# Kernel tuning notes

Hardware: AMD Instinct MI355X
Metric: run time of the kernel (lower is better)

The kernel has to match this reference:

```python
import jax, jax.numpy as jnp
import numpy as np

N = 20000      # nodes
E = 320000     # edges (before self-loops)
IN, HID, H, OUT = 256, 64, 8, 16
NEG_SLOPE = 0.2  # PyG GATConv default


def _gat_layer(x, src, dst, W, a_src, a_dst, b, heads, ch, concat):
    """One PyG-style GATConv (eval mode, self-loops already in src/dst).
    x: [N, F_in]; W: [F_in, heads*ch]; a_src/a_dst: [heads, ch]; b: bias."""
    n = x.shape[0]
    h = (x @ W).reshape(n, heads, ch)                      # [N, H, C]
    alpha_src = jnp.sum(h * a_src, axis=-1)                # [N, H]
    alpha_dst = jnp.sum(h * a_dst, axis=-1)                # [N, H]
    e = jax.nn.leaky_relu(alpha_src[src] + alpha_dst[dst], NEG_SLOPE)  # [Et, H]
    # segment softmax over incoming edges of each dst node (numerically stable)
    m = jax.ops.segment_max(e, dst, num_segments=n)
    m = jnp.where(jnp.isfinite(m), m, 0.0)
    ex = jnp.exp(e - m[dst])
    denom = jax.ops.segment_sum(ex, dst, num_segments=n)
    alpha = ex / jnp.maximum(denom[dst], 1e-16)            # [Et, H]
    # message = alpha * h[src], scatter-add to dst
    out = jax.ops.segment_sum(alpha[:, :, None] * h[src], dst, num_segments=n)  # [N,H,C]
    out = out.reshape(n, heads * ch) if concat else out.mean(axis=1)
    return out + b


def setup_inputs() -> dict:
    key = jax.random.key(0)
    ks = jax.random.split(key, 16)
    p = lambda k, shape, fan: (jax.random.normal(k, shape, jnp.float32) / np.float32(np.sqrt(fan)))
    return {
        "x": jax.random.normal(ks[0], (N, IN), jnp.float32),
        "edge_index": jax.random.randint(ks[1], (2, E), 0, N, dtype=jnp.int32),
        "W1": p(ks[2], (IN, H * HID), IN),
        "a_src1": p(ks[3], (H, HID), HID), "a_dst1": p(ks[4], (H, HID), HID),
        "b1": jnp.zeros((H * HID,), jnp.float32),
        "W2": p(ks[5], (H * HID, H * HID), H * HID),
        "a_src2": p(ks[6], (H, HID), HID), "a_dst2": p(ks[7], (H, HID), HID),
        "b2": jnp.zeros((H * HID,), jnp.float32),
        "W3": p(ks[8], (H * HID, OUT), H * HID),
        "a_src3": p(ks[9], (1, OUT), OUT), "a_dst3": p(ks[10], (1, OUT), OUT),
        "b3": jnp.zeros((OUT,), jnp.float32),
    }


def reference(x, edge_index, W1, a_src1, a_dst1, b1, W2, a_src2, a_dst2, b2,
              W3, a_src3, a_dst3, b3):
    # add self-loops once (PyG GATConv default add_self_loops=True)
    loops = jnp.arange(N, dtype=edge_index.dtype)
    src = jnp.concatenate([edge_index[0], loops])
    dst = jnp.concatenate([edge_index[1], loops])
    h = _gat_layer(x, src, dst, W1, a_src1, a_dst1, b1, H, HID, True)
    h = jax.nn.elu(h)
    h = _gat_layer(h, src, dst, W2, a_src2, a_dst2, b2, H, HID, True)
    h = jax.nn.elu(h)
    h = _gat_layer(h, src, dst, W3, a_src3, a_dst3, b3, 1, OUT, False)
    return jax.nn.log_softmax(h, axis=1)
```

## Files before the change

### kernel.cpp

```cpp
#include <hip/hip_runtime.h>
#include <hip/hip_fp8.h>

#define NEG_SLOPE 0.2f

typedef _Float16 f16x8 __attribute__((ext_vector_type(8)));
typedef float f32x4 __attribute__((ext_vector_type(4)));
typedef float f32x2 __attribute__((ext_vector_type(2)));

#if defined(__has_builtin)
#if __has_builtin(__builtin_amdgcn_cvt_pk_f32_fp8)
#define HAVE_PK_F32_FP8 1
#endif
#if __has_builtin(__builtin_amdgcn_cvt_pk_fp8_f32)
#define HAVE_PK_FP8_F32 1
#endif
#endif

__device__ __forceinline__ float lrelu(float x){ return x >= 0.0f ? x : NEG_SLOPE * x; }
__device__ __forceinline__ float elu1(float x){ return x > 0.0f ? x : __expf(x) - 1.0f; }

__device__ __forceinline__ void gload_lds16(const _Float16* g, _Float16* l){
  __builtin_amdgcn_global_load_lds(
      (const __attribute__((address_space(1))) unsigned int*)g,
      (__attribute__((address_space(3))) unsigned int*)l, 16, 0, 0);
}

__device__ __forceinline__ float f8_to_f32(unsigned char b){
  __hip_fp8_e4m3 t; t.__x = (__hip_fp8_storage_t)b; return (float)t;
}

__device__ __forceinline__ void dq8(uint2 u, float* f){
#ifdef HAVE_PK_F32_FP8
  f32x2 a = __builtin_amdgcn_cvt_pk_f32_fp8(u.x, false);
  f32x2 b = __builtin_amdgcn_cvt_pk_f32_fp8(u.x, true);
  f32x2 c = __builtin_amdgcn_cvt_pk_f32_fp8(u.y, false);
  f32x2 d = __builtin_amdgcn_cvt_pk_f32_fp8(u.y, true);
  f[0]=a[0]; f[1]=a[1]; f[2]=b[0]; f[3]=b[1];
  f[4]=c[0]; f[5]=c[1]; f[6]=d[0]; f[7]=d[1];
#else
  const unsigned char* p = (const unsigned char*)&u;
  #pragma unroll
  for (int j = 0; j < 8; ++j) f[j] = f8_to_f32(p[j]);
#endif
}

__device__ __forceinline__ unsigned int pack4_fp8(float v0, float v1, float v2, float v3){
#ifdef HAVE_PK_FP8_F32
  int pk = __builtin_amdgcn_cvt_pk_fp8_f32(v0, v1, 0, false);
  pk = __builtin_amdgcn_cvt_pk_fp8_f32(v2, v3, pk, true);
  return (unsigned int)pk;
#else
  __hip_fp8_e4m3 q0(v0), q1(v1), q2(v2), q3(v3);
  return (unsigned int)q0.__x | ((unsigned int)q1.__x << 8) |
         ((unsigned int)q2.__x << 16) | ((unsigned int)q3.__x << 24);
#endif
}

union H8U { uint4 u; _Float16 h[8]; };
union P2U { _Float16 h[2]; unsigned int u; };

__global__ __launch_bounds__(256) void prep_kernel(
    const float* __restrict__ x, _Float16* __restrict__ x16, int cvtb, int valid, int total,
    const float* __restrict__ W1, _Float16* __restrict__ W1T,
    const float* __restrict__ W2, _Float16* __restrict__ W2T,
    const int* __restrict__ dstp, int E, int N, int* __restrict__ counts)
{
  __shared__ float tile[32][33];
  int b = blockIdx.x;
  const int tid = threadIdx.x;
  if (b < cvtb){
    int i = (b * 256 + tid) * 8;
    if (i < total){
      H8U o;
      if (i + 8 <= valid){
        float4 v0 = *(const float4*)(x + i);
        float4 v1 = *(const float4*)(x + i + 4);
        o.h[0] = (_Float16)v0.x; o.h[1] = (_Float16)v0.y; o.h[2] = (_Float16)v0.z; o.h[3] = (_Float16)v0.w;
        o.h[4] = (_Float16)v1.x; o.h[5] = (_Float16)v1.y; o.h[6] = (_Float16)v1.z; o.h[7] = (_Float16)v1.w;
      } else {
        #pragma unroll
        for (int j = 0; j < 8; ++j) o.h[j] = (i + j < valid) ? (_Float16)x[i + j] : (_Float16)0.0f;
      }
      *(uint4*)(x16 + i) = o.u;
    }
    return;
  }
  b -= cvtb;
  if (b < 128 + 256){
    const float* W; _Float16* WT; int K, Nn, bb;
    if (b < 128){ W = W1; WT = W1T; K = 256; Nn = 512; bb = b; }
    else        { W = W2; WT = W2T; K = 512; Nn = 512; bb = b - 128; }
    const int nbk = K / 32;
    const int k0 = (bb % nbk) * 32, n0 = (bb / nbk) * 32;
    const int tx = tid & 31, ty = tid >> 5;
    for (int i = ty; i < 32; i += 8)
      tile[i][tx] = W[(size_t)(k0 + i) * Nn + n0 + tx];
    __syncthreads();
    for (int i = ty; i < 32; i += 8)
      WT[(size_t)(n0 + i) * K + k0 + tx] = (_Float16)tile[tx][i];
    return;
  }
  b -= 384;
  {
    int i = b * 256 + tid;
    if (i < E + N){
      int d = (i < E) ? dstp[i] : (i - E);
      atomicAdd(&counts[d], 1);
    }
  }
}

__global__ __launch_bounds__(256) void block_sum_kernel(const int* __restrict__ counts, int N, int* __restrict__ bsum){
  __shared__ int ws[4];
  const int lane = threadIdx.x & 63, wave = threadIdx.x >> 6;
  int i = blockIdx.x * 256 + threadIdx.x;
  int v = (i < N) ? counts[i] : 0;
  #pragma unroll
  for (int msk = 1; msk < 64; msk <<= 1) v += __shfl_xor(v, msk);
  if (lane == 0) ws[wave] = v;
  __syncthreads();
  if (threadIdx.x == 0) bsum[blockIdx.x] = ws[0] + ws[1] + ws[2] + ws[3];
}

__global__ __launch_bounds__(256) void scan_bsum_kernel(int* __restrict__ bsum, int nb, int* __restrict__ offsets, int N){
  __shared__ int tmp[256];
  const int t = threadIdx.x;
  int v = (t < nb) ? bsum[t] : 0;
  tmp[t] = v;
  __syncthreads();
  #pragma unroll
  for (int ofs = 1; ofs < 256; ofs <<= 1){
    int add = (t >= ofs) ? tmp[t - ofs] : 0;
    __syncthreads();
    tmp[t] += add;
    __syncthreads();
  }
  if (t < nb) bsum[t] = tmp[t] - v;
  if (t == nb - 1) offsets[N] = tmp[t];
}

__global__ __launch_bounds__(256) void scan_within_kernel(const int* __restrict__ counts, const int* __restrict__ bsum,
                                                          int* __restrict__ offsets, int N){
  __shared__ int wsum[4];
  const int lane = threadIdx.x & 63, wave = threadIdx.x >> 6;
  int i = blockIdx.x * 256 + threadIdx.x;
  int v = (i < N) ? counts[i] : 0;
  int sc = v;
  #pragma unroll
  for (int ofs = 1; ofs < 64; ofs <<= 1){
    int t = __shfl_up(sc, ofs);
    if (lane >= ofs) sc += t;
  }
  if (lane == 63) wsum[wave] = sc;
  __syncthreads();
  int woff = 0;
  #pragma unroll
  for (int w = 0; w < 4; ++w) if (w < wave) woff += wsum[w];
  if (i < N) offsets[i] = bsum[blockIdx.x] + woff + sc - v;
}

__global__ void fill_kernel(const int* __restrict__ src, const int* __restrict__ dst, int E, int N,
                            const int* __restrict__ offsets, int* __restrict__ cursor, int* __restrict__ csr_src){
  int i = blockIdx.x * blockDim.x + threadIdx.x;
  if (i < E + N){
    int s, d;
    if (i < E){ s = src[i]; d = dst[i]; } else { s = i - E; d = i - E; }
    int pos = atomicAdd(&cursor[d], 1);
    csr_src[offsets[d] + pos] = s;
  }
}

__global__ __launch_bounds__(256) void gemm_f16_mfma_q(
    const _Float16* __restrict__ A, const _Float16* __restrict__ BT,
    unsigned char* __restrict__ H8, float2* __restrict__ ASC,
    const float* __restrict__ a_src, const float* __restrict__ a_dst,
    float* __restrict__ AD,
    int M, int Nn, int K)
{
  __shared__ _Float16 As[64 * 64];
  __shared__ _Float16 Bs[128 * 64];
  const int tid = threadIdx.x;
  const int lane = tid & 63;
  const int wave = tid >> 6;
  const int wr = wave >> 1, wc = wave & 1;
  const int row0 = blockIdx.x * 64;
  const int col0 = blockIdx.y * 128;
  const int r15 = lane & 15;
  const int kgrp = lane >> 4;
  const int head = 2 * blockIdx.y + wc;
  const int sw = r15 & 7;

  f32x4 acc[2][4];
  #pragma unroll
  for (int m = 0; m < 2; ++m)
    #pragma unroll
    for (int n = 0; n < 4; ++n)
      acc[m][n] = (f32x4){0.f, 0.f, 0.f, 0.f};

  for (int k0 = 0; k0 < K; k0 += 64){
    #pragma unroll
    for (int it = 0; it < 2; ++it){
      int ci = it * 256 + tid;
      int r = ci >> 3, ch = (ci & 7) ^ (r & 7);
      gload_lds16(A + (size_t)(row0 + r) * K + k0 + ch * 8, &As[ci * 8]);
    }
    #pragma unroll
    for (int it = 0; it < 4; ++it){
      int ci = it * 256 + tid;
      int r = ci >> 3, ch = (ci & 7) ^ (r & 7);
      gload_lds16(BT + (size_t)(col0 + r) * K + k0 + ch * 8, &Bs[ci * 8]);
    }
    __syncthreads();
    #pragma unroll
    for (int kk = 0; kk < 2; ++kk){
      f16x8 av[2], bv[4];
      #pragma unroll
      for (int q = 0; q < 2; ++q){
        int rr = wr * 32 + q * 16 + r15;
        av[q] = *(const f16x8*)&As[rr * 64 + (((kgrp + kk * 4) ^ sw) * 8)];
      }
      #pragma unroll
      for (int q = 0; q < 4; ++q){
        int rr = wc * 64 + q * 16 + r15;
        bv[q] = *(const f16x8*)&Bs[rr * 64 + (((kgrp + kk * 4) ^ sw) * 8)];
      }
      #pragma unroll
      for (int m = 0; m < 2; ++m)
        #pragma unroll
        for (int n = 0; n < 4; ++n)
          acc[m][n] = __builtin_amdgcn_mfma_f32_16x16x32_f16(av[m], bv[n], acc[m][n], 0, 0, 0);
    }
    __syncthreads();
  }

  float asv[4], adv[4];
  #pragma unroll
  for (int n = 0; n < 4; ++n){
    asv[n] = a_src[head * 64 + n * 16 + r15];
    adv[n] = a_dst[head * 64 + n * 16 + r15];
  }
  #pragma unroll
  for (int m = 0; m < 2; ++m){
    #pragma unroll
    for (int j = 0; j < 4; ++j){
      float ps = 0.f, pd = 0.f, a = 0.f;
      #pragma unroll
      for (int n = 0; n < 4; ++n){
        float c = acc[m][n][j];
        ps += c * asv[n];
        pd += c * adv[n];
        a = fmaxf(a, fabsf(c));
      }
      #pragma unroll
      for (int msk = 1; msk < 16; msk <<= 1){
        ps += __shfl_xor(ps, msk);
        pd += __shfl_xor(pd, msk);
        a = fmaxf(a, __shfl_xor(a, msk));
      }
      float inv = (a > 1e-30f) ? (448.0f / a) : 0.0f;
      int row = row0 + wr * 32 + m * 16 + kgrp * 4 + j;
      unsigned int pk = pack4_fp8(acc[m][0][j] * inv, acc[m][1][j] * inv,
                                  acc[m][2][j] * inv, acc[m][3][j] * inv);
      *(unsigned int*)(H8 + (size_t)row * 512 + head * 64 + r15 * 4) = pk;
      if (r15 == 0 && row < M){
        ASC[(size_t)row * 8 + head] = make_float2(ps, a * (1.0f / 448.0f));
        AD[(size_t)row * 8 + head] = pd;
      }
    }
  }
}

__global__ __launch_bounds__(128) void agg_f8(
    const unsigned char* __restrict__ H8, const float2* __restrict__ ASC,
    const float* __restrict__ AD,
    const int* __restrict__ offsets, const int* __restrict__ csr_src,
    const float* __restrict__ bias, _Float16* __restrict__ O16, int N)
{
  const int wave = threadIdx.x >> 6, lane = threadIdx.x & 63;
  const int d = blockIdx.x * 2 + wave;
  if (d >= N) return;
  const int beg = offsets[d], end = offsets[d + 1];
  const int hA = lane >> 3;
  const int l3 = lane & 7;
  const float aH = AD[(size_t)d * 8 + hA];

  float acc[8];
  #pragma unroll
  for (int j = 0; j < 8; ++j) acc[j] = 0.f;
  float den = 0.f;
  const unsigned char* Hb = H8 + lane * 8;
  int slot = beg;
  for (; slot + 4 <= end; slot += 4){
    int s[4]; float2 pc[4]; uint2 u[4];
    #pragma unroll
    for (int q = 0; q < 4; ++q) s[q] = csr_src[slot + q];
    #pragma unroll
    for (int q = 0; q < 4; ++q) pc[q] = ASC[(size_t)s[q] * 8 + hA];
    #pragma unroll
    for (int q = 0; q < 4; ++q) u[q] = *(const uint2*)(Hb + (size_t)s[q] * 512);
    #pragma unroll
    for (int q = 0; q < 4; ++q){
      float e = __expf(fminf(lrelu(pc[q].x + aH), 60.0f));
      den += e;
      float w = e * pc[q].y;
      float f[8];
      dq8(u[q], f);
      #pragma unroll
      for (int j = 0; j < 8; ++j) acc[j] += w * f[j];
    }
  }
  for (; slot < end; ++slot){
    int s0 = csr_src[slot];
    float2 pc = ASC[(size_t)s0 * 8 + hA];
    uint2 u0 = *(const uint2*)(Hb + (size_t)s0 * 512);
    float e = __expf(fminf(lrelu(pc.x + aH), 60.0f));
    den += e;
    float w = e * pc.y;
    float f[8];
    dq8(u0, f);
    #pragma unroll
    for (int j = 0; j < 8; ++j) acc[j] += w * f[j];
  }

  const float di = 1.0f / fmaxf(den, 1e-16f);
  _Float16* Ob = O16 + (size_t)d * 512 + hA * 64 + 2 * l3;
  const float* Bb = bias + hA * 64 + 2 * l3;
  #pragma unroll
  for (int j = 0; j < 4; ++j){
    float2 bv = *(const float2*)(Bb + j * 16);
    P2U P;
    P.h[0] = (_Float16)elu1(acc[j] * di + bv.x);
    P.h[1] = (_Float16)elu1(acc[j + 4] * di + bv.y);
    *(unsigned int*)(Ob + j * 16) = P.u;
  }
}

__global__ __launch_bounds__(256) void gemm_n16_f16(const _Float16* __restrict__ X, const float* __restrict__ W,
                                                    float* __restrict__ Y,
                                                    const float* __restrict__ a3s, const float* __restrict__ a3d,
                                                    float* __restrict__ AS3, float* __restrict__ AD3,
                                                    int M, int K){
  __shared__ float Ws[512 * 16];
  __shared__ float Xs[64][68];
  const int tid = threadIdx.x;
  for (int i = tid; i < K * 16; i += 256) Ws[i] = W[i];
  const int tx = tid & 15;
  const int ty = tid >> 4;
  const int row0 = blockIdx.x * 64;
  float acc[4] = {0.f, 0.f, 0.f, 0.f};
  for (int k0 = 0; k0 < K; k0 += 64){
    __syncthreads();
    #pragma unroll
    for (int it = 0; it < 2; ++it){
      int idx = it * 2048 + tid * 8;
      int r = idx >> 6, c = idx & 63;
      H8U U; U.u = *(const uint4*)(X + (size_t)(row0 + r) * K + k0 + c);
      float4 f0 = make_float4((float)U.h[0], (float)U.h[1], (float)U.h[2], (float)U.h[3]);
      float4 f1 = make_float4((float)U.h[4], (float)U.h[5], (float)U.h[6], (float)U.h[7]);
      *(float4*)&Xs[r][c] = f0;
      *(float4*)&Xs[r][c + 4] = f1;
    }
    __syncthreads();
    #pragma unroll
    for (int kk = 0; kk < 64; ++kk){
      float w = Ws[(k0 + kk) * 16 + tx];
      #pragma unroll
      for (int i = 0; i < 4; ++i) acc[i] += Xs[ty * 4 + i][kk] * w;
    }
  }
  const float sc = a3s[tx], dc = a3d[tx];
  #pragma unroll
  for (int i = 0; i < 4; ++i){
    int grow = row0 + ty * 4 + i;
    if (grow < M) Y[(size_t)grow * 16 + tx] = acc[i];
    float ps = acc[i] * sc, pd = acc[i] * dc;
    #pragma unroll
    for (int msk = 1; msk < 16; msk <<= 1){
      ps += __shfl_xor(ps, msk);
      pd += __shfl_xor(pd, msk);
    }
    if (tx == 0 && grow < M){ AS3[grow] = ps; AD3[grow] = pd; }
  }
}

__global__ __launch_bounds__(256) void agg3_kernel(
    const float* __restrict__ H3,
    const float* __restrict__ AS3, const float* __restrict__ AD3,
    const int* __restrict__ offsets, const int* __restrict__ csr_src,
    const float* __restrict__ bias, float* __restrict__ Out, int N)
{
  const int wave = threadIdx.x >> 6, lane = threadIdx.x & 63;
  const int d = blockIdx.x * 4 + wave;
  if (d >= N) return;
  const int beg = offsets[d], end = offsets[d + 1];
  const float adv = AD3[d];
  const int c = lane & 15;
  float acc = 0.f, den = 0.f;
  for (int slot = beg + (lane >> 4); slot < end; slot += 4){
    int s = csr_src[slot];
    float e = __expf(fminf(lrelu(AS3[s] + adv), 60.0f));
    den += e;
    acc += e * H3[(size_t)s * 16 + c];
  }
  acc += __shfl_xor(acc, 16);
  acc += __shfl_xor(acc, 32);
  den += __shfl_xor(den, 16);
  den += __shfl_xor(den, 32);
  float v = acc / fmaxf(den, 1e-16f) + bias[c];
  float mm = v;
  #pragma unroll
  for (int msk = 1; msk < 16; msk <<= 1) mm = fmaxf(mm, __shfl_xor(mm, msk));
  float se = __expf(v - mm);
  #pragma unroll
  for (int msk = 1; msk < 16; msk <<= 1) se += __shfl_xor(se, msk);
  float r = v - mm - __logf(se);
  if (lane < 16) Out[(size_t)d * 16 + lane] = r;
}

extern "C" void kernel_launch(void* const* d_in, const int* in_sizes, int n_in,
                              void* d_out, int out_size, void* d_ws, size_t ws_size,
                              hipStream_t stream)
{
  const float* x   = (const float*)d_in[0];
  const int*   ei  = (const int*)d_in[1];
  const float* W1  = (const float*)d_in[2];
  const float* as1 = (const float*)d_in[3];
  const float* ad1 = (const float*)d_in[4];
  const float* b1  = (const float*)d_in[5];
  const float* W2  = (const float*)d_in[6];
  const float* as2 = (const float*)d_in[7];
  const float* ad2 = (const float*)d_in[8];
  const float* b2  = (const float*)d_in[9];
  const float* W3  = (const float*)d_in[10];
  const float* as3 = (const float*)d_in[11];
  const float* ad3 = (const float*)d_in[12];
  const float* b3  = (const float*)d_in[13];

  const int N    = in_sizes[0] / 256;
  const int E    = in_sizes[1] / 2;
  const int Et   = E + N;
  const int Mpad = (N + 127) & ~127;
  const int nb   = (N + 255) / 256;
  const int* src = ei;
  const int* dst = ei + E;

  char* base = (char*)d_ws;
  size_t off = 0;
  auto take = [&](size_t bytes) -> char* {
    char* p = base + off;
    off = (off + bytes + 255) & ~(size_t)255;
    return p;
  };
  _Float16* x16  = (_Float16*)take((size_t)Mpad * 256 * 2);
  _Float16* O16  = (_Float16*)take((size_t)Mpad * 512 * 2);
  unsigned char* H8 = (unsigned char*)take((size_t)Mpad * 512);
  float2* ASC = (float2*)take((size_t)Mpad * 8 * 8);
  _Float16* W1T  = (_Float16*)take((size_t)512 * 256 * 2);
  _Float16* W2T  = (_Float16*)take((size_t)512 * 512 * 2);
  float* AD   = (float*)take((size_t)Mpad * 8 * 4);
  float* H3   = (float*)take((size_t)N * 16 * 4);
  float* AS3  = (float*)take((size_t)N * 4);
  float* AD3  = (float*)take((size_t)N * 4);
  int* counts  = (int*)take((size_t)2 * N * 4);
  int* cursor  = counts + N;
  int* offsets = (int*)take((size_t)(N + 1) * 4);
  int* bsum    = (int*)take((size_t)(nb + 1) * 4);
  int* csr     = (int*)take((size_t)Et * 4);
  if (off > ws_size) return;

  hipMemsetAsync(counts, 0, (size_t)2 * N * 4, stream);
  const int tb = 256;
  const int cvtb = Mpad / 8;
  const int cntb = (Et + tb - 1) / tb;
  prep_kernel<<<cvtb + 384 + cntb, tb, 0, stream>>>(
      x, x16, cvtb, N * 256, Mpad * 256, W1, W1T, W2, W2T, dst, E, N, counts);
  block_sum_kernel<<<nb, 256, 0, stream>>>(counts, N, bsum);
  scan_bsum_kernel<<<1, 256, 0, stream>>>(bsum, nb, offsets, N);
  scan_within_kernel<<<nb, 256, 0, stream>>>(counts, bsum, offsets, N);
  fill_kernel<<<(Et + tb - 1) / tb, tb, 0, stream>>>(src, dst, E, N, offsets, cursor, csr);

  const int gM = Mpad / 64;
  gemm_f16_mfma_q<<<dim3(gM, 4), 256, 0, stream>>>(x16, W1T, H8, ASC, as1, ad1, AD, N, 512, 256);
  agg_f8<<<(N + 1) / 2, 128, 0, stream>>>(H8, ASC, AD, offsets, csr, b1, O16, N);
  gemm_f16_mfma_q<<<dim3(gM, 4), 256, 0, stream>>>(O16, W2T, H8, ASC, as2, ad2, AD, N, 512, 512);
  agg_f8<<<(N + 1) / 2, 128, 0, stream>>>(H8, ASC, AD, offsets, csr, b2, O16, N);
  gemm_n16_f16<<<(N + 63) / 64, 256, 0, stream>>>(O16, W3, H3, as3, ad3, AS3, AD3, N, 512);
  agg3_kernel<<<(N + 3) / 4, 256, 0, stream>>>(H3, AS3, AD3, offsets, csr, b3, (float*)d_out, N);
}
```

Measured before the change: 200.3 us.

## Fuse fp32-to-fp16 input conversion into first GEMM and merge scan kernels

The standalone conversion of x to fp16 is removed. The first GEMM instead reads fp32 rows and converts them while writing to LDS, via a template flag. The block-sum and block-offset scan kernels are merged into one kernel, where the last block to finish does the scan, found through an atomic counter and fences. This removes an intermediate buffer round-trip and a kernel launch. In exchange, each column block re-reads wider fp32 input and loses the asynchronous global-to-LDS load path.

```diff
diff --git a/kernel.cpp b/kernel.cpp
--- a/kernel.cpp
+++ b/kernel.cpp
@@ -60,7 +60,6 @@
 union P2U { _Float16 h[2]; unsigned int u; };
 
 __global__ __launch_bounds__(256) void prep_kernel(
-    const float* __restrict__ x, _Float16* __restrict__ x16, int cvtb, int valid, int total,
     const float* __restrict__ W1, _Float16* __restrict__ W1T,
     const float* __restrict__ W2, _Float16* __restrict__ W2T,
     const int* __restrict__ dstp, int E, int N, int* __restrict__ counts)
@@ -68,24 +67,6 @@
   __shared__ float tile[32][33];
   int b = blockIdx.x;
   const int tid = threadIdx.x;
-  if (b < cvtb){
-    int i = (b * 256 + tid) * 8;
-    if (i < total){
-      H8U o;
-      if (i + 8 <= valid){
-        float4 v0 = *(const float4*)(x + i);
-        float4 v1 = *(const float4*)(x + i + 4);
-        o.h[0] = (_Float16)v0.x; o.h[1] = (_Float16)v0.y; o.h[2] = (_Float16)v0.z; o.h[3] = (_Float16)v0.w;
-        o.h[4] = (_Float16)v1.x; o.h[5] = (_Float16)v1.y; o.h[6] = (_Float16)v1.z; o.h[7] = (_Float16)v1.w;
-      } else {
-        #pragma unroll
-        for (int j = 0; j < 8; ++j) o.h[j] = (i + j < valid) ? (_Float16)x[i + j] : (_Float16)0.0f;
-      }
-      *(uint4*)(x16 + i) = o.u;
-    }
-    return;
-  }
-  b -= cvtb;
   if (b < 128 + 256){
     const float* W; _Float16* WT; int K, Nn, bb;
     if (b < 128){ W = W1; WT = W1T; K = 256; Nn = 512; bb = b; }
@@ -110,33 +91,43 @@
   }
 }
 
-__global__ __launch_bounds__(256) void block_sum_kernel(const int* __restrict__ counts, int N, int* __restrict__ bsum){
+__global__ __launch_bounds__(256) void sumscan_kernel(const int* __restrict__ counts, int N, int nb,
+                                                      int* __restrict__ bsum, int* __restrict__ offsets,
+                                                      int* __restrict__ done){
   __shared__ int ws[4];
+  __shared__ int is_last;
+  __shared__ int tmp[256];
   const int lane = threadIdx.x & 63, wave = threadIdx.x >> 6;
   int i = blockIdx.x * 256 + threadIdx.x;
   int v = (i < N) ? counts[i] : 0;
-  #pragma unroll
-  for (int msk = 1; msk < 64; msk <<= 1) v += __shfl_xor(v, msk);
-  if (lane == 0) ws[wave] = v;
+  int sv = v;
+  #pragma unroll
+  for (int msk = 1; msk < 64; msk <<= 1) sv += __shfl_xor(sv, msk);
+  if (lane == 0) ws[wave] = sv;
   __syncthreads();
-  if (threadIdx.x == 0) bsum[blockIdx.x] = ws[0] + ws[1] + ws[2] + ws[3];
-}
-
-__global__ __launch_bounds__(256) void scan_bsum_kernel(int* __restrict__ bsum, int nb, int* __restrict__ offsets, int N){
-  __shared__ int tmp[256];
-  const int t = threadIdx.x;
-  int v = (t < nb) ? bsum[t] : 0;
-  tmp[t] = v;
+  if (threadIdx.x == 0){
+    bsum[blockIdx.x] = ws[0] + ws[1] + ws[2] + ws[3];
+    __threadfence();
+    int old = atomicAdd(done, 1);
+    is_last = (old == nb - 1);
+  }
   __syncthreads();
-  #pragma unroll
-  for (int ofs = 1; ofs < 256; ofs <<= 1){
-    int add = (t >= ofs) ? tmp[t - ofs] : 0;
+  if (is_last){
+    __threadfence();
+    const int t = threadIdx.x;
+    int b = (t < nb) ? bsum[t] : 0;
+    tmp[t] = b;
     __syncthreads();
-    tmp[t] += add;
-    __syncthreads();
-  }
-  if (t < nb) bsum[t] = tmp[t] - v;
-  if (t == nb - 1) offsets[N] = tmp[t];
+    #pragma unroll
+    for (int ofs = 1; ofs < 256; ofs <<= 1){
+      int add = (t >= ofs) ? tmp[t - ofs] : 0;
+      __syncthreads();
+      tmp[t] += add;
+      __syncthreads();
+    }
+    if (t < nb) bsum[t] = tmp[t] - b;
+    if (t == nb - 1) offsets[N] = tmp[t];
+  }
 }
 
 __global__ __launch_bounds__(256) void scan_within_kernel(const int* __restrict__ counts, const int* __restrict__ bsum,
@@ -170,8 +161,9 @@
   }
 }
 
+template<int AF32>
 __global__ __launch_bounds__(256) void gemm_f16_mfma_q(
-    const _Float16* __restrict__ A, const _Float16* __restrict__ BT,
+    const void* __restrict__ Av, const _Float16* __restrict__ BT,
     unsigned char* __restrict__ H8, float2* __restrict__ ASC,
     const float* __restrict__ a_src, const float* __restrict__ a_dst,
     float* __restrict__ AD,
@@ -198,11 +190,33 @@
       acc[m][n] = (f32x4){0.f, 0.f, 0.f, 0.f};
 
   for (int k0 = 0; k0 < K; k0 += 64){
-    #pragma unroll
-    for (int it = 0; it < 2; ++it){
-      int ci = it * 256 + tid;
-      int r = ci >> 3, ch = (ci & 7) ^ (r & 7);
-      gload_lds16(A + (size_t)(row0 + r) * K + k0 + ch * 8, &As[ci * 8]);
+    if (AF32){
+      const float* Af = (const float*)Av;
+      #pragma unroll
+      for (int it = 0; it < 2; ++it){
+        int ci = it * 256 + tid;
+        int r = ci >> 3, ch = (ci & 7) ^ (r & 7);
+        f16x8 h;
+        if (row0 + r < M){
+          const float* ap = Af + (size_t)(row0 + r) * K + k0 + ch * 8;
+          float4 f0 = *(const float4*)ap;
+          float4 f1 = *(const float4*)(ap + 4);
+          h[0]=(_Float16)f0.x; h[1]=(_Float16)f0.y; h[2]=(_Float16)f0.z; h[3]=(_Float16)f0.w;
+          h[4]=(_Float16)f1.x; h[5]=(_Float16)f1.y; h[6]=(_Float16)f1.z; h[7]=(_Float16)f1.w;
+        } else {
+          #pragma unroll
+          for (int j = 0; j < 8; ++j) h[j] = (_Float16)0.0f;
+        }
+        *(f16x8*)&As[ci * 8] = h;
+      }
+    } else {
+      const _Float16* Ah = (const _Float16*)Av;
+      #pragma unroll
+      for (int it = 0; it < 2; ++it){
+        int ci = it * 256 + tid;
+        int r = ci >> 3, ch = (ci & 7) ^ (r & 7);
+        gload_lds16(Ah + (size_t)(row0 + r) * K + k0 + ch * 8, &As[ci * 8]);
+      }
     }
     #pragma unroll
     for (int it = 0; it < 4; ++it){
@@ -451,7 +465,6 @@
     off = (off + bytes + 255) & ~(size_t)255;
     return p;
   };
-  _Float16* x16  = (_Float16*)take((size_t)Mpad * 256 * 2);
   _Float16* O16  = (_Float16*)take((size_t)Mpad * 512 * 2);
   unsigned char* H8 = (unsigned char*)take((size_t)Mpad * 512);
   float2* ASC = (float2*)take((size_t)Mpad * 8 * 8);
@@ -461,28 +474,26 @@
   float* H3   = (float*)take((size_t)N * 16 * 4);
   float* AS3  = (float*)take((size_t)N * 4);
   float* AD3  = (float*)take((size_t)N * 4);
-  int* counts  = (int*)take((size_t)2 * N * 4);
+  int* counts  = (int*)take((size_t)(2 * N + 1) * 4);
   int* cursor  = counts + N;
+  int* done    = counts + 2 * N;
   int* offsets = (int*)take((size_t)(N + 1) * 4);
   int* bsum    = (int*)take((size_t)(nb + 1) * 4);
   int* csr     = (int*)take((size_t)Et * 4);
   if (off > ws_size) return;
 
-  hipMemsetAsync(counts, 0, (size_t)2 * N * 4, stream);
+  hipMemsetAsync(counts, 0, (size_t)(2 * N + 1) * 4, stream);
   const int tb = 256;
-  const int cvtb = Mpad / 8;
   const int cntb = (Et + tb - 1) / tb;
-  prep_kernel<<<cvtb + 384 + cntb, tb, 0, stream>>>(
-      x, x16, cvtb, N * 256, Mpad * 256, W1, W1T, W2, W2T, dst, E, N, counts);
-  block_sum_kernel<<<nb, 256, 0, stream>>>(counts, N, bsum);
-  scan_bsum_kernel<<<1, 256, 0, stream>>>(bsum, nb, offsets, N);
+  prep_kernel<<<384 + cntb, tb, 0, stream>>>(W1, W1T, W2, W2T, dst, E, N, counts);
+  sumscan_kernel<<<nb, 256, 0, stream>>>(counts, N, nb, bsum, offsets, done);
   scan_within_kernel<<<nb, 256, 0, stream>>>(counts, bsum, offsets, N);
   fill_kernel<<<(Et + tb - 1) / tb, tb, 0, stream>>>(src, dst, E, N, offsets, cursor, csr);
 
   const int gM = Mpad / 64;
-  gemm_f16_mfma_q<<<dim3(gM, 4), 256, 0, stream>>>(x16, W1T, H8, ASC, as1, ad1, AD, N, 512, 256);
+  gemm_f16_mfma_q<1><<<dim3(gM, 4), 256, 0, stream>>>(x, W1T, H8, ASC, as1, ad1, AD, N, 512, 256);
   agg_f8<<<(N + 1) / 2, 128, 0, stream>>>(H8, ASC, AD, offsets, csr, b1, O16, N);
-  gemm_f16_mfma_q<<<dim3(gM, 4), 256, 0, stream>>>(O16, W2T, H8, ASC, as2, ad2, AD, N, 512, 512);
+  gemm_f16_mfma_q<0><<<dim3(gM, 4), 256, 0, stream>>>(O16, W2T, H8, ASC, as2, ad2, AD, N, 512, 512);
   agg_f8<<<(N + 1) / 2, 128, 0, stream>>>(H8, ASC, AD, offsets, csr, b2, O16, N);
   gemm_n16_f16<<<(N + 63) / 64, 256, 0, stream>>>(O16, W3, H3, as3, ad3, AS3, AD3, N, 512);
   agg3_kernel<<<(N + 3) / 4, 256, 0, stream>>>(H3, AS3, AD3, offsets, csr, b3, (float*)d_out, N);
```

After: 207.5 us. 1.04x slower.
